# Optimization experiments

Hardware: AMD Instinct MI355X
Metric: run time of the kernel (lower is better)

## Reference

```python
import jax, jax.numpy as jnp
import numpy as np


def setup_inputs() -> dict:
    key = jax.random.key(0)
    k1, k2, k3 = jax.random.split(key, 3)
    B, H, W = 32, 512, 512
    N = H * W  # tokens
    K = 32768  # positive_trials
    decision_scores = jax.random.normal(k1, (B, N, 2), dtype=jnp.float32)
    s_map = jax.random.uniform(k2, (B, 1, H, W), dtype=jnp.float32)
    # uniform noise for gumbel sampling, kept away from {0,1} for log stability
    u = jax.random.uniform(k3, (B, N, 2), dtype=jnp.float32, minval=1e-6, maxval=1.0 - 1e-6)
    return {"decision_scores": decision_scores, "s_map": s_map, "u": u, "positive_trials": K}


def reference(decision_scores, s_map, u, positive_trials):
    B, N, _ = decision_scores.shape
    # gumbel_softmax(hard=False, tau=1): softmax(logits + gumbel_noise)
    gumbel = -jnp.log(-jnp.log(u))
    logp = jax.nn.log_softmax(decision_scores + gumbel, axis=-1)  # [B, N, 2]
    # soft_decisions = p[..., 0]
    # Tokenizer: [B, 1, H, W] -> [B, N, 1]; use channel 0 as salience score.
    scores = s_map.reshape(B, 1, -1).transpose(0, 2, 1)[..., 0]  # [B, N]
    # argsort descending, take top-k indices == lax.top_k indices
    _, idx = jax.lax.top_k(scores, positive_trials)  # [B, K]
    trials = jnp.zeros((B, N), dtype=decision_scores.dtype)
    trials = trials.at[jnp.arange(B)[:, None], idx].set(1.0)  # scatter ones
    # BCE(sum): -sum(t*log(p) + (1-t)*log(1-p)); with 2-class softmax, 1-p0 = p1.
    # torch BCE clamps log terms at -100.
    logp0 = jnp.clip(logp[..., 0], -100.0)
    logp1 = jnp.clip(logp[..., 1], -100.0)
    loss = -jnp.sum(trials * logp0 + (1.0 - trials) * logp1)
    return loss
```

## Files before the change

### kernel.cpp

```cpp
#include <hip/hip_runtime.h>

#define NB    4096
#define CAP   1024
#define BATCH 32
#define NTOK  262144
#define HB    512
#define HPB   16
#define LOSS_BLOCKS 4096

typedef float floatx4 __attribute__((ext_vector_type(4)));

__device__ __forceinline__ int bucket_of(float v) {
    int b = (int)(v * (float)NB);
    return b > NB - 1 ? NB - 1 : b;
}

__global__ void hist_kernel(const float* __restrict__ smap, int* __restrict__ ghist) {
    __shared__ int lh[NB];
    for (int i = threadIdx.x; i < NB; i += 256) lh[i] = 0;
    __syncthreads();
    const int b  = blockIdx.x / HPB;
    const int cb = blockIdx.x % HPB;
    const int chunk = NTOK / HPB;
    const float4* src = (const float4*)(smap + (size_t)b * NTOK + (size_t)cb * chunk);
    for (int i = threadIdx.x; i < chunk / 4; i += 256) {
        float4 v = src[i];
        atomicAdd(&lh[bucket_of(v.x)], 1);
        atomicAdd(&lh[bucket_of(v.y)], 1);
        atomicAdd(&lh[bucket_of(v.z)], 1);
        atomicAdd(&lh[bucket_of(v.w)], 1);
    }
    __syncthreads();
    int* out = ghist + (size_t)blockIdx.x * NB;
    for (int i = threadIdx.x; i < NB; i += 256) out[i] = lh[i];
}

__global__ __launch_bounds__(1024) void select_kernel(const int* __restrict__ ghist,
                                                      const int* __restrict__ kptr,
                                                      int* __restrict__ tbR,
                                                      int* __restrict__ cnt) {
    __shared__ int hist[NB];
    __shared__ int sA[1024];
    __shared__ int sB[1024];
    const int tid = threadIdx.x;
    const int b   = blockIdx.x;
    if (tid == 0) cnt[b] = 0;

    const int C = NB / 1024;
    int base = tid * C;
    const int* gh0 = ghist + (size_t)b * HPB * NB;
#pragma unroll
    for (int i = 0; i < C; i++) {
        int s = 0;
        for (int c = 0; c < HPB; c++) s += gh0[c * NB + base + i];
        hist[base + i] = s;
    }
    int csum = hist[base] + hist[base + 1] + hist[base + 2] + hist[base + 3];
    sA[tid] = csum;
    __syncthreads();

    int* pin = sA; int* pout = sB;
    for (int st = 1; st < 1024; st <<= 1) {
        int v = pin[tid] + ((tid + st < 1024) ? pin[tid + st] : 0);
        pout[tid] = v;
        __syncthreads();
        int* t_ = pin; pin = pout; pout = t_;
    }
    int above = (tid < 1023) ? pin[tid + 1] : 0;

    const int K = *kptr;
    int cum = above;
    for (int i = C - 1; i >= 0; i--) {
        int hb = hist[base + i];
        if (cum < K && cum + hb >= K) {
            tbR[2 * b]     = base + i;
            tbR[2 * b + 1] = K - cum;
        }
        cum += hb;
    }
}

__global__ void collect_kernel(const float* __restrict__ smap, const int* __restrict__ tbR,
                               int* __restrict__ cnt, float* __restrict__ cval,
                               int* __restrict__ cidx) {
    const int cbpb = 8;
    const int b  = blockIdx.x / cbpb;
    const int cb = blockIdx.x % cbpb;
    const int chunk = NTOK / cbpb;
    const int tb = tbR[2 * b];
    const float4* src = (const float4*)(smap + (size_t)b * NTOK + (size_t)cb * chunk);
    const int base_n = cb * chunk;
    for (int i = threadIdx.x; i < chunk / 4; i += 256) {
        float4 v = src[i];
        float vals[4] = {v.x, v.y, v.z, v.w};
#pragma unroll
        for (int s = 0; s < 4; s++) {
            if (bucket_of(vals[s]) == tb) {
                int p = atomicAdd(&cnt[b], 1);
                if (p < CAP) {
                    cval[b * CAP + p] = vals[s];
                    cidx[b * CAP + p] = base_n + 4 * i + s;
                }
            }
        }
    }
}

__global__ void refine_kernel(const int* __restrict__ tbR, const int* __restrict__ cnt,
                              const float* __restrict__ cval, const int* __restrict__ cidx,
                              float* __restrict__ T, int* __restrict__ ncut) {
    const int b = blockIdx.x;
    const int R = tbR[2 * b + 1];
    int M = cnt[b];
    bool ovf = (M > CAP);
    if (M > CAP) M = CAP;
    __shared__ float sv[CAP];
    __shared__ int   si[CAP];
    for (int i = threadIdx.x; i < M; i += 256) {
        sv[i] = cval[b * CAP + i];
        si[i] = cidx[b * CAP + i];
    }
    __syncthreads();
    if (ovf || R > M || R < 1) {
        if (threadIdx.x == 0) { T[b] = (float)tbR[2 * b] / (float)NB; ncut[b] = 0x7fffffff; }
        return;
    }
    for (int i = threadIdx.x; i < M; i += 256) {
        float vi = sv[i]; int ii = si[i];
        int r = 0;
        for (int j = 0; j < M; j++) {
            float vj = sv[j];
            r += (vj > vi) || (vj == vi && si[j] < ii);
        }
        if (r == R - 1) { T[b] = vi; ncut[b] = ii; }
    }
}

__device__ __forceinline__ float token_loss(float d0, float d1, float u0, float u1,
                                            bool sel) {
    float g0 = -__logf(-__logf(u0));
    float g1 = -__logf(-__logf(u1));
    float dd = (d0 + g0) - (d1 + g1);
    float l  = __logf(1.f + __expf(-fabsf(dd)));
    float lp0 = (dd >= 0.f) ? -l      : dd - l;
    float lp1 = (dd >= 0.f) ? -l - dd : -l;
    lp0 = fmaxf(lp0, -100.f); lp1 = fmaxf(lp1, -100.f);
    return sel ? -lp0 : -lp1;
}

__global__ void loss_kernel(const float* __restrict__ ds, const float* __restrict__ u,
                            const float* __restrict__ smap, const float* __restrict__ T,
                            const int* __restrict__ ncut, float* __restrict__ partials) {
    int tid = blockIdx.x * blockDim.x + threadIdx.x;
    int b  = tid >> 15;
    int p8 = tid & 32767;
    const floatx4* ds4 = (const floatx4*)(ds + (size_t)b * NTOK * 2);
    const floatx4* u4  = (const floatx4*)(u  + (size_t)b * NTOK * 2);
    const float4*  s4  = (const float4*)(smap + (size_t)b * NTOK);

    floatx4 d0 = __builtin_nontemporal_load(&ds4[4 * p8 + 0]);
    floatx4 d1 = __builtin_nontemporal_load(&ds4[4 * p8 + 1]);
    floatx4 d2 = __builtin_nontemporal_load(&ds4[4 * p8 + 2]);
    floatx4 d3 = __builtin_nontemporal_load(&ds4[4 * p8 + 3]);
    floatx4 u0 = __builtin_nontemporal_load(&u4[4 * p8 + 0]);
    floatx4 u1 = __builtin_nontemporal_load(&u4[4 * p8 + 1]);
    floatx4 u2 = __builtin_nontemporal_load(&u4[4 * p8 + 2]);
    floatx4 u3 = __builtin_nontemporal_load(&u4[4 * p8 + 3]);
    float4 sa = s4[2 * p8 + 0];
    float4 sb = s4[2 * p8 + 1];

    float Tb = T[b];
    int   nc = ncut[b];
    int   n0 = p8 << 3;

    bool e0 = (sa.x > Tb) || (sa.x == Tb && (n0 + 0) <= nc);
    bool e1 = (sa.y > Tb) || (sa.y == Tb && (n0 + 1) <= nc);
    bool e2 = (sa.z > Tb) || (sa.z == Tb && (n0 + 2) <= nc);
    bool e3 = (sa.w > Tb) || (sa.w == Tb && (n0 + 3) <= nc);
    bool e4 = (sb.x > Tb) || (sb.x == Tb && (n0 + 4) <= nc);
    bool e5 = (sb.y > Tb) || (sb.y == Tb && (n0 + 5) <= nc);
    bool e6 = (sb.z > Tb) || (sb.z == Tb && (n0 + 6) <= nc);
    bool e7 = (sb.w > Tb) || (sb.w == Tb && (n0 + 7) <= nc);

    float acc = token_loss(d0.x, d0.y, u0.x, u0.y, e0)
              + token_loss(d0.z, d0.w, u0.z, u0.w, e1)
              + token_loss(d1.x, d1.y, u1.x, u1.y, e2)
              + token_loss(d1.z, d1.w, u1.z, u1.w, e3)
              + token_loss(d2.x, d2.y, u2.x, u2.y, e4)
              + token_loss(d2.z, d2.w, u2.z, u2.w, e5)
              + token_loss(d3.x, d3.y, u3.x, u3.y, e6)
              + token_loss(d3.z, d3.w, u3.z, u3.w, e7);

    for (int off = 32; off > 0; off >>= 1) acc += __shfl_down(acc, off, 64);
    __shared__ float red[4];
    int lane = threadIdx.x & 63, wv = threadIdx.x >> 6;
    if (lane == 0) red[wv] = acc;
    __syncthreads();
    if (threadIdx.x == 0)
        partials[blockIdx.x] = red[0] + red[1] + red[2] + red[3];
}

__global__ void reduce_kernel(const float* __restrict__ partials, float* __restrict__ out) {
    float acc = 0.f;
    for (int i = threadIdx.x; i < LOSS_BLOCKS; i += blockDim.x) acc += partials[i];
    for (int off = 32; off > 0; off >>= 1) acc += __shfl_down(acc, off, 64);
    __shared__ float red[16];
    int lane = threadIdx.x & 63, wv = threadIdx.x >> 6;
    if (lane == 0) red[wv] = acc;
    __syncthreads();
    if (threadIdx.x == 0) {
        float s = 0.f;
        for (int w = 0; w < (int)(blockDim.x >> 6); w++) s += red[w];
        out[0] = s;
    }
}

extern "C" void kernel_launch(void* const* d_in, const int* in_sizes, int n_in,
                              void* d_out, int out_size, void* d_ws, size_t ws_size,
                              hipStream_t stream) {
    const float* ds   = (const float*)d_in[0];
    const float* smap = (const float*)d_in[1];
    const float* u    = (const float*)d_in[2];
    const int*   kptr = (const int*)d_in[3];

    int*   ghist = (int*)d_ws;
    int*   cnt   = ghist + HB * NB;
    int*   tbR   = cnt + BATCH;
    float* T     = (float*)(tbR + 2 * BATCH);
    int*   ncut  = (int*)(T + BATCH);
    float* cval  = (float*)(ncut + BATCH);
    int*   cidx  = (int*)(cval + BATCH * CAP);
    float* partials = (float*)(cidx + BATCH * CAP);

    hist_kernel<<<HB, 256, 0, stream>>>(smap, ghist);
    select_kernel<<<BATCH, 1024, 0, stream>>>(ghist, kptr, tbR, cnt);
    collect_kernel<<<256, 256, 0, stream>>>(smap, tbR, cnt, cval, cidx);
    refine_kernel<<<BATCH, 256, 0, stream>>>(tbR, cnt, cval, cidx, T, ncut);
    loss_kernel<<<LOSS_BLOCKS, 256, 0, stream>>>(ds, u, smap, T, ncut, partials);
    reduce_kernel<<<1, 1024, 0, stream>>>(partials, (float*)d_out);
}
```

Before: 213.1 us.

## Merge per-block histograms atomically, widen collect grid, process 16 tokens per loss thread

The hist kernel now adds its shared histogram into one per-batch global histogram with atomics, after a memset, instead of writing sixteen partial histograms that select then sums. This cuts the global traffic and the select kernel's reduction loop. The collect kernel now uses 16 chunks per batch instead of 8, giving more blocks. The loss kernel handles 16 tokens per thread with half as many blocks, which raises memory-level parallelism per thread but uses more registers and gives fewer waves.

```diff
diff --git a/kernel.cpp b/kernel.cpp
--- a/kernel.cpp
+++ b/kernel.cpp
@@ -6,7 +6,7 @@
 #define NTOK  262144
 #define HB    512
 #define HPB   16
-#define LOSS_BLOCKS 4096
+#define LOSS_BLOCKS 2048
 
 typedef float floatx4 __attribute__((ext_vector_type(4)));
 
@@ -15,7 +15,7 @@
     return b > NB - 1 ? NB - 1 : b;
 }
 
-__global__ void hist_kernel(const float* __restrict__ smap, int* __restrict__ ghist) {
+__global__ void hist_kernel(const float* __restrict__ smap, int* __restrict__ hist) {
     __shared__ int lh[NB];
     for (int i = threadIdx.x; i < NB; i += 256) lh[i] = 0;
     __syncthreads();
@@ -31,15 +31,18 @@
         atomicAdd(&lh[bucket_of(v.w)], 1);
     }
     __syncthreads();
-    int* out = ghist + (size_t)blockIdx.x * NB;
-    for (int i = threadIdx.x; i < NB; i += 256) out[i] = lh[i];
-}
-
-__global__ __launch_bounds__(1024) void select_kernel(const int* __restrict__ ghist,
+    int* gh = hist + b * NB;
+    for (int i = threadIdx.x; i < NB; i += 256) {
+        int c = lh[i];
+        if (c) atomicAdd(&gh[i], c);
+    }
+}
+
+__global__ __launch_bounds__(1024) void select_kernel(const int* __restrict__ hist,
                                                       const int* __restrict__ kptr,
                                                       int* __restrict__ tbR,
                                                       int* __restrict__ cnt) {
-    __shared__ int hist[NB];
+    __shared__ int h[NB];
     __shared__ int sA[1024];
     __shared__ int sB[1024];
     const int tid = threadIdx.x;
@@ -48,14 +51,10 @@
 
     const int C = NB / 1024;
     int base = tid * C;
-    const int* gh0 = ghist + (size_t)b * HPB * NB;
-#pragma unroll
-    for (int i = 0; i < C; i++) {
-        int s = 0;
-        for (int c = 0; c < HPB; c++) s += gh0[c * NB + base + i];
-        hist[base + i] = s;
-    }
-    int csum = hist[base] + hist[base + 1] + hist[base + 2] + hist[base + 3];
+    const int* gh = hist + b * NB;
+#pragma unroll
+    for (int i = 0; i < C; i++) h[base + i] = gh[base + i];
+    int csum = h[base] + h[base + 1] + h[base + 2] + h[base + 3];
     sA[tid] = csum;
     __syncthreads();
 
@@ -71,7 +70,7 @@
     const int K = *kptr;
     int cum = above;
     for (int i = C - 1; i >= 0; i--) {
-        int hb = hist[base + i];
+        int hb = h[base + i];
         if (cum < K && cum + hb >= K) {
             tbR[2 * b]     = base + i;
             tbR[2 * b + 1] = K - cum;
@@ -83,10 +82,9 @@
 __global__ void collect_kernel(const float* __restrict__ smap, const int* __restrict__ tbR,
                                int* __restrict__ cnt, float* __restrict__ cval,
                                int* __restrict__ cidx) {
-    const int cbpb = 8;
-    const int b  = blockIdx.x / cbpb;
-    const int cb = blockIdx.x % cbpb;
-    const int chunk = NTOK / cbpb;
+    const int b  = blockIdx.x / HPB;
+    const int cb = blockIdx.x % HPB;
+    const int chunk = NTOK / HPB;
     const int tb = tbR[2 * b];
     const float4* src = (const float4*)(smap + (size_t)b * NTOK + (size_t)cb * chunk);
     const int base_n = cb * chunk;
@@ -152,44 +150,35 @@
                             const float* __restrict__ smap, const float* __restrict__ T,
                             const int* __restrict__ ncut, float* __restrict__ partials) {
     int tid = blockIdx.x * blockDim.x + threadIdx.x;
-    int b  = tid >> 15;
-    int p8 = tid & 32767;
+    int b   = tid >> 14;
+    int p16 = tid & 16383;
     const floatx4* ds4 = (const floatx4*)(ds + (size_t)b * NTOK * 2);
     const floatx4* u4  = (const floatx4*)(u  + (size_t)b * NTOK * 2);
     const float4*  s4  = (const float4*)(smap + (size_t)b * NTOK);
 
-    floatx4 d0 = __builtin_nontemporal_load(&ds4[4 * p8 + 0]);
-    floatx4 d1 = __builtin_nontemporal_load(&ds4[4 * p8 + 1]);
-    floatx4 d2 = __builtin_nontemporal_load(&ds4[4 * p8 + 2]);
-    floatx4 d3 = __builtin_nontemporal_load(&ds4[4 * p8 + 3]);
-    floatx4 u0 = __builtin_nontemporal_load(&u4[4 * p8 + 0]);
-    floatx4 u1 = __builtin_nontemporal_load(&u4[4 * p8 + 1]);
-    floatx4 u2 = __builtin_nontemporal_load(&u4[4 * p8 + 2]);
-    floatx4 u3 = __builtin_nontemporal_load(&u4[4 * p8 + 3]);
-    float4 sa = s4[2 * p8 + 0];
-    float4 sb = s4[2 * p8 + 1];
-
-    float Tb = T[b];
-    int   nc = ncut[b];
-    int   n0 = p8 << 3;
-
-    bool e0 = (sa.x > Tb) || (sa.x == Tb && (n0 + 0) <= nc);
-    bool e1 = (sa.y > Tb) || (sa.y == Tb && (n0 + 1) <= nc);
-    bool e2 = (sa.z > Tb) || (sa.z == Tb && (n0 + 2) <= nc);
-    bool e3 = (sa.w > Tb) || (sa.w == Tb && (n0 + 3) <= nc);
-    bool e4 = (sb.x > Tb) || (sb.x == Tb && (n0 + 4) <= nc);
-    bool e5 = (sb.y > Tb) || (sb.y == Tb && (n0 + 5) <= nc);
-    bool e6 = (sb.z > Tb) || (sb.z == Tb && (n0 + 6) <= nc);
-    bool e7 = (sb.w > Tb) || (sb.w == Tb && (n0 + 7) <= nc);
-
-    float acc = token_loss(d0.x, d0.y, u0.x, u0.y, e0)
-              + token_loss(d0.z, d0.w, u0.z, u0.w, e1)
-              + token_loss(d1.x, d1.y, u1.x, u1.y, e2)
-              + token_loss(d1.z, d1.w, u1.z, u1.w, e3)
-              + token_loss(d2.x, d2.y, u2.x, u2.y, e4)
-              + token_loss(d2.z, d2.w, u2.z, u2.w, e5)
-              + token_loss(d3.x, d3.y, u3.x, u3.y, e6)
-              + token_loss(d3.z, d3.w, u3.z, u3.w, e7);
+    floatx4 dv[8], uv[8];
+    float4  sm[4];
+#pragma unroll
+    for (int j = 0; j < 8; j++) dv[j] = __builtin_nontemporal_load(&ds4[8 * p16 + j]);
+#pragma unroll
+    for (int j = 0; j < 8; j++) uv[j] = __builtin_nontemporal_load(&u4[8 * p16 + j]);
+#pragma unroll
+    for (int j = 0; j < 4; j++) sm[j] = s4[4 * p16 + j];
+
+    const float Tb = T[b];
+    const int   nc = ncut[b];
+    const int   n0 = p16 << 4;
+    const float* smf = (const float*)sm;
+
+    float acc = 0.f;
+#pragma unroll
+    for (int j = 0; j < 8; j++) {
+        float v0 = smf[2 * j], v1 = smf[2 * j + 1];
+        bool sel0 = (v0 > Tb) || (v0 == Tb && (n0 + 2 * j)     <= nc);
+        bool sel1 = (v1 > Tb) || (v1 == Tb && (n0 + 2 * j + 1) <= nc);
+        acc += token_loss(dv[j].x, dv[j].y, uv[j].x, uv[j].y, sel0)
+             + token_loss(dv[j].z, dv[j].w, uv[j].z, uv[j].w, sel1);
+    }
 
     for (int off = 32; off > 0; off >>= 1) acc += __shfl_down(acc, off, 64);
     __shared__ float red[4];
@@ -223,18 +212,19 @@
     const float* u    = (const float*)d_in[2];
     const int*   kptr = (const int*)d_in[3];
 
-    int*   ghist = (int*)d_ws;
-    int*   cnt   = ghist + HB * NB;
-    int*   tbR   = cnt + BATCH;
-    float* T     = (float*)(tbR + 2 * BATCH);
-    int*   ncut  = (int*)(T + BATCH);
-    float* cval  = (float*)(ncut + BATCH);
-    int*   cidx  = (int*)(cval + BATCH * CAP);
+    int*   hist = (int*)d_ws;
+    int*   cnt  = hist + BATCH * NB;
+    int*   tbR  = cnt + BATCH;
+    float* T    = (float*)(tbR + 2 * BATCH);
+    int*   ncut = (int*)(T + BATCH);
+    float* cval = (float*)(ncut + BATCH);
+    int*   cidx = (int*)(cval + BATCH * CAP);
     float* partials = (float*)(cidx + BATCH * CAP);
 
-    hist_kernel<<<HB, 256, 0, stream>>>(smap, ghist);
-    select_kernel<<<BATCH, 1024, 0, stream>>>(ghist, kptr, tbR, cnt);
-    collect_kernel<<<256, 256, 0, stream>>>(smap, tbR, cnt, cval, cidx);
+    hipMemsetAsync(hist, 0, (size_t)(BATCH * NB) * sizeof(int), stream);
+    hist_kernel<<<HB, 256, 0, stream>>>(smap, hist);
+    select_kernel<<<BATCH, 1024, 0, stream>>>(hist, kptr, tbR, cnt);
+    collect_kernel<<<HB, 256, 0, stream>>>(smap, tbR, cnt, cval, cidx);
     refine_kernel<<<BATCH, 256, 0, stream>>>(tbR, cnt, cval, cidx, T, ncut);
     loss_kernel<<<LOSS_BLOCKS, 256, 0, stream>>>(ds, u, smap, T, ncut, partials);
     reduce_kernel<<<1, 1024, 0, stream>>>(partials, (float*)d_out);
```

Result: slower. 237.5 us (+11.5%).
